# Optimization experiments

Hardware: AMD Instinct MI355X
Metric: run time of the kernel (lower is better)

The kernel has to match this reference:

```python
import jax, jax.numpy as jnp
import numpy as np

EPS = 1e-05


def layer_norm(x, scale):
    # Faithful to source bug: returns scale * x_norm + scale (shift param unused)
    mean = jnp.mean(x, axis=-1, keepdims=True)
    var = jnp.var(x, axis=-1, keepdims=True)  # unbiased=False
    x_norm = (x - mean) / jnp.sqrt(var + EPS)
    return scale * x_norm + scale


def mhsa(x, wq, wk, wv, wo, bo, n_heads):
    b, t, d = x.shape
    hd = d // n_heads
    # torch Linear: y = x @ W.T (no qkv bias)
    q = (x @ wq.T).reshape(b, t, n_heads, hd).transpose(0, 2, 1, 3)  # bhtd
    k = (x @ wk.T).reshape(b, t, n_heads, hd).transpose(0, 2, 1, 3)
    v = (x @ wv.T).reshape(b, t, n_heads, hd).transpose(0, 2, 1, 3)
    scores = jnp.einsum('bhqd,bhkd->bhqk', q, k)
    causal = jnp.triu(jnp.ones((t, t), dtype=bool), k=1)
    scores = jnp.where(causal, -jnp.inf, scores)
    attn = jax.nn.softmax(scores / np.sqrt(hd).astype(np.float32), axis=-1)
    ctx = jnp.einsum('bhqk,bhkd->bhqd', attn, v)
    ctx = ctx.transpose(0, 2, 1, 3).reshape(b, t, d)
    return ctx @ wo.T + bo


def setup_inputs() -> dict:
    key = jax.random.key(0)
    ks = jax.random.split(key, 6)
    B, T, D = 2, 2048, 1024
    return {
        'x': jax.random.normal(ks[0], (B, T, D), dtype=jnp.float32),
        'wq': jax.random.normal(ks[1], (D, D), dtype=jnp.float32) * 0.02,
        'wk': jax.random.normal(ks[2], (D, D), dtype=jnp.float32) * 0.02,
        'wv': jax.random.normal(ks[3], (D, D), dtype=jnp.float32) * 0.02,
        'wo': jax.random.normal(ks[4], (D, D), dtype=jnp.float32) * 0.02,
        'bo': jnp.zeros((D,), dtype=jnp.float32),
        'ln1_scale': jnp.ones((D,), dtype=jnp.float32),
        'ln2_scale': jnp.ones((D,), dtype=jnp.float32),
    }


def reference(x, wq, wk, wv, wo, bo, ln1_scale, ln2_scale):
    n_heads = 16
    # Block 1: norm1 -> attn -> (+residual); dropout is identity in eval mode
    h = x + mhsa(layer_norm(x, ln1_scale), wq, wk, wv, wo, bo, n_heads)
    # Block 2: source calls self.attn (same weights) again, not self.ff
    out = h + mhsa(layer_norm(h, ln2_scale), wq, wk, wv, wo, bo, n_heads)
    return out
```

## Files before the change

### kernel.cpp

```cpp
#include <hip/hip_runtime.h>
#include <hip/hip_bf16.h>
#include <math.h>

#define Dm 1024
#define Tm 2048
#define Bm 2
#define Hm 16
#define HDm 64
#define Rm (Bm*Tm)
#define QKS 2048

typedef __attribute__((ext_vector_type(8))) short sh8;
typedef __attribute__((ext_vector_type(4))) float f32x4;
typedef __attribute__((ext_vector_type(16))) float f32x16;

#define AS1(p) ((const __attribute__((address_space(1))) void*)(p))
#define AS3(p) ((__attribute__((address_space(3))) void*)(p))

__device__ __forceinline__ short f2bs(float f) {
    union { float f; unsigned u; } v; v.f = f;
    unsigned r = v.u + 0x7FFFu + ((v.u >> 16) & 1u);
    return (short)(r >> 16);
}

__global__ __launch_bounds__(256) void ln_conv(const float* __restrict__ x,
                                               const float* __restrict__ scale,
                                               short* __restrict__ out,
                                               const float* __restrict__ wq,
                                               const float* __restrict__ wk,
                                               const float* __restrict__ wv,
                                               const float* __restrict__ wo,
                                               short* __restrict__ wqkv,
                                               short* __restrict__ wob) {
    __shared__ float red[8];
    if (blockIdx.x >= 4096) {
        int idx = ((blockIdx.x - 4096) * 256 + threadIdx.x) * 4;
        const int M1 = 1 << 20;
        const float* src; short* dst; int off; float sc = 1.0f;
        if (idx < M1)           { src = wq; dst = wqkv;          off = idx; sc = 0.125f; }
        else if (idx < 2*M1)    { src = wk; dst = wqkv + M1;     off = idx - M1; }
        else if (idx < 3*M1)    { src = wv; dst = wqkv + 2*M1;   off = idx - 2*M1; }
        else                    { src = wo; dst = wob;           off = idx - 3*M1; }
        float4 v = *(const float4*)(src + off);
        short4 o;
        o.x = f2bs(v.x*sc); o.y = f2bs(v.y*sc); o.z = f2bs(v.z*sc); o.w = f2bs(v.w*sc);
        *(short4*)(dst + off) = o;
        return;
    }
    int row = blockIdx.x;
    int t = threadIdx.x;
    const float4* xr = (const float4*)(x + (size_t)row * Dm);
    float4 v = xr[t];
    float s  = v.x + v.y + v.z + v.w;
    float ss = v.x*v.x + v.y*v.y + v.z*v.z + v.w*v.w;
    #pragma unroll
    for (int off = 32; off; off >>= 1) {
        s  += __shfl_xor(s, off);
        ss += __shfl_xor(ss, off);
    }
    int wave = t >> 6, lane = t & 63;
    if (lane == 0) { red[wave*2] = s; red[wave*2+1] = ss; }
    __syncthreads();
    s  = red[0] + red[2] + red[4] + red[6];
    ss = red[1] + red[3] + red[5] + red[7];
    float mean = s * (1.0f / Dm);
    float var  = ss * (1.0f / Dm) - mean * mean;
    float rstd = 1.0f / sqrtf(var + 1e-5f);
    float4 sc = ((const float4*)scale)[t];
    short4 o;
    o.x = f2bs(sc.x * ((v.x - mean) * rstd) + sc.x);
    o.y = f2bs(sc.y * ((v.y - mean) * rstd) + sc.y);
    o.z = f2bs(sc.z * ((v.z - mean) * rstd) + sc.z);
    o.w = f2bs(sc.w * ((v.w - mean) * rstd) + sc.w);
    ((short4*)(out + (size_t)row * Dm))[t] = o;
}

__global__ __launch_bounds__(256) void ln_kernel(const float* __restrict__ x,
                                                 const float* __restrict__ scale,
                                                 short* __restrict__ out) {
    int row = blockIdx.x;
    int t = threadIdx.x;
    const float4* xr = (const float4*)(x + (size_t)row * Dm);
    float4 v = xr[t];
    float s  = v.x + v.y + v.z + v.w;
    float ss = v.x*v.x + v.y*v.y + v.z*v.z + v.w*v.w;
    #pragma unroll
    for (int off = 32; off; off >>= 1) {
        s  += __shfl_xor(s, off);
        ss += __shfl_xor(ss, off);
    }
    __shared__ float red[8];
    int wave = t >> 6, lane = t & 63;
    if (lane == 0) { red[wave*2] = s; red[wave*2+1] = ss; }
    __syncthreads();
    s  = red[0] + red[2] + red[4] + red[6];
    ss = red[1] + red[3] + red[5] + red[7];
    float mean = s * (1.0f / Dm);
    float var  = ss * (1.0f / Dm) - mean * mean;
    float rstd = 1.0f / sqrtf(var + 1e-5f);
    float4 sc = ((const float4*)scale)[t];
    short4 o;
    o.x = f2bs(sc.x * ((v.x - mean) * rstd) + sc.x);
    o.y = f2bs(sc.y * ((v.y - mean) * rstd) + sc.y);
    o.z = f2bs(sc.z * ((v.z - mean) * rstd) + sc.z);
    o.w = f2bs(sc.w * ((v.w - mean) * rstd) + sc.w);
    ((short4*)(out + (size_t)row * Dm))[t] = o;
}

template<int BN, int MODE>
__global__ __launch_bounds__(256) void gemm_mfma(const short* __restrict__ A,
                                                 const short* __restrict__ B,
                                                 const float* __restrict__ bias,
                                                 const float* __restrict__ res,
                                                 void* __restrict__ Cv,
                                                 short* __restrict__ Vt,
                                                 int M, int N, int K) {
    __shared__ short As[128*64];
    __shared__ short Bs[BN*64];
    __shared__ short Tb[(MODE==1) ? 4*16*68 : 4];
    const int NJ = BN / 32;
    int t = threadIdx.x;
    int lane = t & 63, w = t >> 6;
    int l = lane & 15, quad = lane >> 4;
    int wm = (w & 1) * 64, wn = (w >> 1) * (BN/2);
    int m0 = blockIdx.y * 128, n0 = blockIdx.x * BN;

    f32x4 acc[4][NJ];
    #pragma unroll
    for (int i = 0; i < 4; i++)
        #pragma unroll
        for (int j = 0; j < NJ; j++)
            acc[i][j] = (f32x4){0.f,0.f,0.f,0.f};

    for (int k0 = 0; k0 < K; k0 += 64) {
        __syncthreads();
        #pragma unroll
        for (int p = 0; p < 4; p++) {
            int off = p*4096 + t*16;
            int row = off >> 7;
            int c = ((off >> 4) & 7) ^ (row & 7);
            const short* ga = A + (size_t)(m0 + row) * K + k0 + c*8;
            __builtin_amdgcn_global_load_lds(AS1(ga), AS3((char*)As + off), 16, 0, 0);
        }
        #pragma unroll
        for (int p = 0; p < BN/32; p++) {
            int off = p*4096 + t*16;
            int row = off >> 7;
            int c = ((off >> 4) & 7) ^ (row & 7);
            const short* gb = B + (size_t)(n0 + row) * K + k0 + c*8;
            __builtin_amdgcn_global_load_lds(AS1(gb), AS3((char*)Bs + off), 16, 0, 0);
        }
        __syncthreads();
        sh8 a0[4], a1[4], b0[NJ], b1[NJ];
        #pragma unroll
        for (int i = 0; i < 4; i++) {
            int m = wm + i*16 + l;
            const char* ar = (const char*)As + m*128;
            int sw = m & 7;
            a0[i] = *(const sh8*)(ar + ((quad ^ sw) * 16));
            a1[i] = *(const sh8*)(ar + (((4 + quad) ^ sw) * 16));
        }
        #pragma unroll
        for (int j = 0; j < NJ; j++) {
            int n = wn + j*16 + l;
            const char* br = (const char*)Bs + n*128;
            int sw = n & 7;
            b0[j] = *(const sh8*)(br + ((quad ^ sw) * 16));
            b1[j] = *(const sh8*)(br + (((4 + quad) ^ sw) * 16));
        }
        #pragma unroll
        for (int i = 0; i < 4; i++)
            #pragma unroll
            for (int j = 0; j < NJ; j++) {
                acc[i][j] = __builtin_amdgcn_mfma_f32_16x16x32_bf16(a0[i], b0[j], acc[i][j], 0, 0, 0);
                acc[i][j] = __builtin_amdgcn_mfma_f32_16x16x32_bf16(a1[i], b1[j], acc[i][j], 0, 0, 0);
            }
    }
    if (MODE == 0) {
        #pragma unroll
        for (int i = 0; i < 4; i++)
            #pragma unroll
            for (int j = 0; j < NJ; j++)
                #pragma unroll
                for (int r = 0; r < 4; r++) {
                    int m = m0 + wm + i*16 + quad*4 + r;
                    int n = n0 + wn + j*16 + l;
                    float vv = acc[i][j][r] + bias[n] + res[(size_t)m * N + n];
                    ((float*)Cv)[(size_t)m * N + n] = vv;
                }
    } else {
        if (n0 < 2048) {
            #pragma unroll
            for (int i = 0; i < 4; i++)
                #pragma unroll
                for (int j = 0; j < NJ; j++)
                    #pragma unroll
                    for (int r = 0; r < 4; r++) {
                        int m = m0 + wm + i*16 + quad*4 + r;
                        int n = n0 + wn + j*16 + l;
                        ((short*)Cv)[(size_t)m * QKS + n] = f2bs(acc[i][j][r]);
                    }
        } else {
            int bq = m0 >> 11;
            int key0 = (m0 & 2047) + wm;
            int h = (n0 + wn - 2048) >> 6;
            int quad2 = ((quad & 1) << 1) | (quad >> 1);
            short* vout = Vt + ((size_t)(bq*Hm + h) * HDm) * Tm + key0;
            #pragma unroll
            for (int j = 0; j < NJ; j++) {
                #pragma unroll
                for (int i = 0; i < 4; i++) {
                    short4 o;
                    o.x = f2bs(acc[i][j][0]); o.y = f2bs(acc[i][j][1]);
                    o.z = f2bs(acc[i][j][2]); o.w = f2bs(acc[i][j][3]);
                    *(short4*)&Tb[w*(16*68) + l*68 + i*16 + quad2*4] = o;
                }
                #pragma unroll
                for (int st = 0; st < 2; st++) {
                    int rr = st*8 + (lane >> 3);
                    int cc = lane & 7;
                    sh8 vv = *(const sh8*)&Tb[w*(16*68) + rr*68 + cc*8];
                    *(sh8*)(vout + (size_t)(j*16 + rr) * Tm + cc*8) = vv;
                }
            }
        }
    }
}

__global__ __launch_bounds__(256) void attn_mfma(const short* __restrict__ qk,
                                                 const short* __restrict__ vtg,
                                                 short* __restrict__ ctx) {
    __shared__ short Kl[3][64*64];
    __shared__ short Vl[2][64*64];
    int t = threadIdx.x;
    int lane = t & 63, w = t >> 6;
    int qh = w & 1, kh = w >> 1;
    int l31 = lane & 31, hi = lane >> 5;
    int bh = blockIdx.x;
    int xi = blockIdx.y;
    int cc0 = xi & 7, kk0 = xi >> 3;
    int qt = (kk0 == 0) ? cc0 : (kk0 == 1) ? (15 - cc0)
           : (kk0 == 2) ? (16 + cc0) : (31 - cc0);
    int b = bh >> 4, h = bh & 15;
    size_t rbase = (size_t)b * Tm;
    const short* qp0 = qk + rbase * QKS + h*HDm;
    const short* kp0 = qp0 + Dm;
    const short* vh  = vtg + ((size_t)bh * HDm) * Tm;
    int qtbase = qt * 64;
    int qrow = qtbase + qh*32 + l31;

    sh8 qf[4];
    {
        const short* qp = qp0 + (size_t)qrow * QKS + hi*8;
        qf[0] = *(const sh8*)qp;
        qf[1] = *(const sh8*)(qp + 16);
        qf[2] = *(const sh8*)(qp + 32);
        qf[3] = *(const sh8*)(qp + 48);
    }

    f32x16 O0, O1;
    #pragma unroll
    for (int i = 0; i < 16; i++) { O0[i] = 0.f; O1[i] = 0.f; }
    float ps = 0.f;

    int trow = t >> 3;
    int c8 = ((t & 7) ^ (trow & 7)) * 8;
    int ldsoff = t * 16;
    const short* gkp = kp0 + (size_t)trow * QKS + c8;
    const short* gvp = vh + (size_t)trow * Tm + c8;

#define STAGE_K(KD) do { \
    __builtin_amdgcn_global_load_lds(AS1(gkp),                  AS3((char*)(KD) + ldsoff), 16, 0, 0); \
    __builtin_amdgcn_global_load_lds(AS1(gkp + (size_t)32*QKS), AS3((char*)(KD) + 4096 + ldsoff), 16, 0, 0); \
    gkp += (size_t)64*QKS; } while (0)

#define STAGE_V(VD) do { \
    __builtin_amdgcn_global_load_lds(AS1(gvp),                 AS3((char*)(VD) + ldsoff), 16, 0, 0); \
    __builtin_amdgcn_global_load_lds(AS1(gvp + (size_t)32*Tm), AS3((char*)(VD) + 4096 + ldsoff), 16, 0, 0); \
    gvp += 64; } while (0)

#define QKCOMP(KBUF) do { \
    const char* kr_ = (const char*)(KBUF) + (kh*32 + l31)*128; \
    int sw_ = l31 & 7; \
    f32x16 c_; \
    _Pragma("unroll") for (int i_ = 0; i_ < 16; i_++) c_[i_] = 0.f; \
    _Pragma("unroll") for (int s_ = 0; s_ < 4; s_++) { \
        sh8 kf_ = *(const sh8*)(kr_ + (((s_*2 + hi) ^ sw_) * 16)); \
        c_ = __builtin_amdgcn_mfma_f32_32x32x16_bf16(kf_, qf[s_], c_, 0, 0, 0); } \
    S0 = c_; \
} while (0)

    STAGE_K(Kl[0]);
    STAGE_V(Vl[0]);
    if (qt >= 1) STAGE_K(Kl[1]);
    __syncthreads();

    f32x16 S0;
    QKCOMP(Kl[0]);

    int bcur = 0;
    for (int kc = 0; kc <= qt; kc++) {
        int kbase = kc * 64;
        sh8 pa[2];
        {
            bool needmask = (kbase + kh*32 + 31 > qtbase + qh*32);
            float p_[16];
            if (needmask) {
                #pragma unroll
                for (int r = 0; r < 16; r++) {
                    int key_r = kbase + kh*32 + (r&3) + 8*(r>>2) + 4*hi;
                    p_[r] = (key_r > qrow) ? 0.f : __expf(S0[r]);
                }
            } else {
                #pragma unroll
                for (int r = 0; r < 16; r++) p_[r] = __expf(S0[r]);
            }
            ps += (((p_[0]+p_[1])+(p_[2]+p_[3])) + ((p_[4]+p_[5])+(p_[6]+p_[7])))
                + (((p_[8]+p_[9])+(p_[10]+p_[11])) + ((p_[12]+p_[13])+(p_[14]+p_[15])));
            #pragma unroll
            for (int gg = 0; gg < 2; gg++) {
                union { __hip_bfloat162 h2[4]; sh8 s8; } u;
                u.h2[0] = __float22bfloat162_rn({p_[gg*8+0], p_[gg*8+1]});
                u.h2[1] = __float22bfloat162_rn({p_[gg*8+2], p_[gg*8+3]});
                u.h2[2] = __float22bfloat162_rn({p_[gg*8+4], p_[gg*8+5]});
                u.h2[3] = __float22bfloat162_rn({p_[gg*8+6], p_[gg*8+7]});
                pa[gg] = u.s8;
            }
        }

        __syncthreads();

        int bnext = (bcur == 2) ? 0 : bcur + 1;
        if (kc + 2 <= qt) {
            int bnext2 = (bnext == 2) ? 0 : bnext + 1;
            STAGE_K(Kl[bnext2]);
        }
        if (kc + 1 <= qt) STAGE_V(Vl[(kc + 1) & 1]);

        if (kc < qt) QKCOMP(Kl[bnext]);

        const char* Vb = (const char*)Vl[kc & 1];
        int G0 = kh * 2;
        {
            const char* vr = Vb + l31*128;
            int sw = l31 & 7;
            sh8 v0 = *(const sh8*)(vr + ((((G0  )*2 + hi) ^ sw) * 16));
            sh8 v1 = *(const sh8*)(vr + ((((G0+1)*2 + hi) ^ sw) * 16));
            O0 = __builtin_amdgcn_mfma_f32_32x32x16_bf16(pa[0], v0, O0, 0, 0, 0);
            O0 = __builtin_amdgcn_mfma_f32_32x32x16_bf16(pa[1], v1, O0, 0, 0, 0);
        }
        {
            const char* vr = Vb + (32 + l31)*128;
            int sw = l31 & 7;
            sh8 v0 = *(const sh8*)(vr + ((((G0  )*2 + hi) ^ sw) * 16));
            sh8 v1 = *(const sh8*)(vr + ((((G0+1)*2 + hi) ^ sw) * 16));
            O1 = __builtin_amdgcn_mfma_f32_32x32x16_bf16(pa[0], v0, O1, 0, 0, 0);
            O1 = __builtin_amdgcn_mfma_f32_32x32x16_bf16(pa[1], v1, O1, 0, 0, 0);
        }
        bcur = bnext;
    }
#undef STAGE_K
#undef STAGE_V
#undef QKCOMP

    ps += __shfl_xor(ps, 32);
    __syncthreads();
    float* Lo  = (float*)Kl;
    float* Lps = (float*)Vl;
    if (kh == 1) {
        #pragma unroll
        for (int r = 0; r < 16; r++) {
            int rl = (r&3) + 8*(r>>2) + 4*hi;
            Lo[qh*2048 + rl*64 + l31]      = O0[r];
            Lo[qh*2048 + rl*64 + 32 + l31] = O1[r];
        }
        if (hi == 0) Lps[qh*32 + l31] = ps;
    }
    __syncthreads();
    if (kh == 0) {
        float pst = ps + Lps[qh*32 + l31];
        float inv_own = 1.0f / pst;
        short* cp = ctx + (rbase + qtbase + qh*32) * Dm + h*HDm + l31;
        #pragma unroll
        for (int r = 0; r < 16; r++) {
            int rl = (r&3) + 8*(r>>2) + 4*hi;
            float inv = __shfl(inv_own, rl);
            cp[(size_t)rl * Dm]      = f2bs((O0[r] + Lo[qh*2048 + rl*64 + l31]) * inv);
            cp[(size_t)rl * Dm + 32] = f2bs((O1[r] + Lo[qh*2048 + rl*64 + 32 + l31]) * inv);
        }
    }
}

extern "C" void kernel_launch(void* const* d_in, const int* in_sizes, int n_in,
                              void* d_out, int out_size, void* d_ws, size_t ws_size,
                              hipStream_t stream) {
    const float* x   = (const float*)d_in[0];
    const float* wq  = (const float*)d_in[1];
    const float* wk  = (const float*)d_in[2];
    const float* wv  = (const float*)d_in[3];
    const float* wo  = (const float*)d_in[4];
    const float* bo  = (const float*)d_in[5];
    const float* ln1 = (const float*)d_in[6];
    const float* ln2 = (const float*)d_in[7];
    float* out = (float*)d_out;

    short* lnb  = (short*)d_ws;
    short* ctxb = lnb  + (size_t)Rm*Dm;
    short* qk   = ctxb + (size_t)Rm*Dm;
    short* vtg  = qk   + (size_t)Rm*QKS;
    short* wqkv = vtg  + (size_t)Bm*Hm*HDm*Tm;
    short* wob  = wqkv + (size_t)3*Dm*Dm;

    dim3 qgrid(3072/128, Rm/128);
    dim3 pgrid(Dm/64,    Rm/128);
    dim3 agrid(32, 32);

    ln_conv<<<8192, 256, 0, stream>>>(x, ln1, lnb, wq, wk, wv, wo, wqkv, wob);
    gemm_mfma<128, 1><<<qgrid, 256, 0, stream>>>(lnb, wqkv, nullptr, nullptr, qk, vtg, Rm, 3072, Dm);
    attn_mfma<<<agrid, 256, 0, stream>>>(qk, vtg, ctxb);
    gemm_mfma<64, 0><<<pgrid, 256, 0, stream>>>(ctxb, wob, bo, x, out, nullptr, Rm, Dm, Dm);

    ln_kernel<<<Rm, 256, 0, stream>>>(out, ln2, lnb);
    gemm_mfma<128, 1><<<qgrid, 256, 0, stream>>>(lnb, wqkv, nullptr, nullptr, qk, vtg, Rm, 3072, Dm);
    attn_mfma<<<agrid, 256, 0, stream>>>(qk, vtg, ctxb);
    gemm_mfma<64, 0><<<pgrid, 256, 0, stream>>>(ctxb, wob, bo, out, out, nullptr, Rm, Dm, Dm);
}
```

Before: 266.8 us.

## Pair complementary causal query tiles per attention block for balanced work

```diff
diff --git a/kernel.cpp b/kernel.cpp
--- a/kernel.cpp
+++ b/kernel.cpp
@@ -231,31 +231,32 @@
                                                  const short* __restrict__ vtg,
                                                  short* __restrict__ ctx) {
     __shared__ short Kl[3][64*64];
-    __shared__ short Vl[2][64*64];
+    __shared__ short Vl[3][64*64];
+    __shared__ float Cb[2][32][64];
+    __shared__ float Cps[64];
     int t = threadIdx.x;
     int lane = t & 63, w = t >> 6;
     int qh = w & 1, kh = w >> 1;
     int l31 = lane & 31, hi = lane >> 5;
     int bh = blockIdx.x;
-    int xi = blockIdx.y;
-    int cc0 = xi & 7, kk0 = xi >> 3;
-    int qt = (kk0 == 0) ? cc0 : (kk0 == 1) ? (15 - cc0)
-           : (kk0 == 2) ? (16 + cc0) : (31 - cc0);
+    int pr = blockIdx.y;
+    int qt0 = pr, qt1 = 31 - pr;
     int b = bh >> 4, h = bh & 15;
     size_t rbase = (size_t)b * Tm;
     const short* qp0 = qk + rbase * QKS + h*HDm;
     const short* kp0 = qp0 + Dm;
     const short* vh  = vtg + ((size_t)bh * HDm) * Tm;
-    int qtbase = qt * 64;
-    int qrow = qtbase + qh*32 + l31;
-
-    sh8 qf[4];
+    int qrow0 = qt0*64 + qh*32 + l31;
+    int qrow1 = qt1*64 + qh*32 + l31;
+
+    sh8 qfA[4], qfB[4];
     {
-        const short* qp = qp0 + (size_t)qrow * QKS + hi*8;
-        qf[0] = *(const sh8*)qp;
-        qf[1] = *(const sh8*)(qp + 16);
-        qf[2] = *(const sh8*)(qp + 32);
-        qf[3] = *(const sh8*)(qp + 48);
+        const short* qp = qp0 + (size_t)qrow0 * QKS + hi*8;
+        qfA[0] = *(const sh8*)qp;       qfA[1] = *(const sh8*)(qp + 16);
+        qfA[2] = *(const sh8*)(qp + 32); qfA[3] = *(const sh8*)(qp + 48);
+        const short* qq = qp0 + (size_t)qrow1 * QKS + hi*8;
+        qfB[0] = *(const sh8*)qq;       qfB[1] = *(const sh8*)(qq + 16);
+        qfB[2] = *(const sh8*)(qq + 32); qfB[3] = *(const sh8*)(qq + 48);
     }
 
     f32x16 O0, O1;
@@ -266,49 +267,76 @@
     int trow = t >> 3;
     int c8 = ((t & 7) ^ (trow & 7)) * 8;
     int ldsoff = t * 16;
-    const short* gkp = kp0 + (size_t)trow * QKS + c8;
-    const short* gvp = vh + (size_t)trow * Tm + c8;
-
-#define STAGE_K(KD) do { \
-    __builtin_amdgcn_global_load_lds(AS1(gkp),                  AS3((char*)(KD) + ldsoff), 16, 0, 0); \
-    __builtin_amdgcn_global_load_lds(AS1(gkp + (size_t)32*QKS), AS3((char*)(KD) + 4096 + ldsoff), 16, 0, 0); \
-    gkp += (size_t)64*QKS; } while (0)
-
-#define STAGE_V(VD) do { \
-    __builtin_amdgcn_global_load_lds(AS1(gvp),                 AS3((char*)(VD) + ldsoff), 16, 0, 0); \
-    __builtin_amdgcn_global_load_lds(AS1(gvp + (size_t)32*Tm), AS3((char*)(VD) + 4096 + ldsoff), 16, 0, 0); \
-    gvp += 64; } while (0)
-
-#define QKCOMP(KBUF) do { \
+    const short* kst = kp0 + (size_t)trow * QKS + c8;
+    const short* vst = vh + (size_t)trow * Tm + c8;
+
+#define KBOF(j) ((((j) <= qt0) ? (j) : ((j) - qt0 - 1)) * 64)
+#define STAGE(j, rg) do { \
+    int kb_ = KBOF(j); \
+    const short* gk_ = kst + (size_t)kb_ * QKS; \
+    const short* gv_ = vst + kb_; \
+    __builtin_amdgcn_global_load_lds(AS1(gk_), AS3((char*)Kl[rg] + ldsoff), 16, 0, 0); \
+    __builtin_amdgcn_global_load_lds(AS1(gk_ + (size_t)32*QKS), AS3((char*)Kl[rg] + 4096 + ldsoff), 16, 0, 0); \
+    __builtin_amdgcn_global_load_lds(AS1(gv_), AS3((char*)Vl[rg] + ldsoff), 16, 0, 0); \
+    __builtin_amdgcn_global_load_lds(AS1(gv_ + (size_t)32*Tm), AS3((char*)Vl[rg] + 4096 + ldsoff), 16, 0, 0); \
+} while (0)
+
+#define QKCOMP(KBUF, QF) do { \
     const char* kr_ = (const char*)(KBUF) + (kh*32 + l31)*128; \
     int sw_ = l31 & 7; \
     f32x16 c_; \
     _Pragma("unroll") for (int i_ = 0; i_ < 16; i_++) c_[i_] = 0.f; \
     _Pragma("unroll") for (int s_ = 0; s_ < 4; s_++) { \
         sh8 kf_ = *(const sh8*)(kr_ + (((s_*2 + hi) ^ sw_) * 16)); \
-        c_ = __builtin_amdgcn_mfma_f32_32x32x16_bf16(kf_, qf[s_], c_, 0, 0, 0); } \
+        c_ = __builtin_amdgcn_mfma_f32_32x32x16_bf16(kf_, QF[s_], c_, 0, 0, 0); } \
     S0 = c_; \
 } while (0)
 
-    STAGE_K(Kl[0]);
-    STAGE_V(Vl[0]);
-    if (qt >= 1) STAGE_K(Kl[1]);
+#define EPI(QTB) do { \
+    ps += __shfl_xor(ps, 32); \
+    if (kh == 1) { \
+        _Pragma("unroll") for (int r_ = 0; r_ < 16; r_++) { \
+            int rl_ = (r_&3) + 8*(r_>>2) + 4*hi; \
+            Cb[qh][rl_][l31]      = O0[r_]; \
+            Cb[qh][rl_][32 + l31] = O1[r_]; \
+        } \
+        if (hi == 0) Cps[qh*32 + l31] = ps; \
+    } \
+    __syncthreads(); \
+    if (kh == 0) { \
+        float pst_ = ps + Cps[qh*32 + l31]; \
+        float invo_ = 1.0f / pst_; \
+        short* cp_ = ctx + (rbase + (QTB) + qh*32) * Dm + h*HDm + l31; \
+        _Pragma("unroll") for (int r_ = 0; r_ < 16; r_++) { \
+            int rl_ = (r_&3) + 8*(r_>>2) + 4*hi; \
+            float inv_ = __shfl(invo_, rl_); \
+            cp_[(size_t)rl_ * Dm]      = f2bs((O0[r_] + Cb[qh][rl_][l31]) * inv_); \
+            cp_[(size_t)rl_ * Dm + 32] = f2bs((O1[r_] + Cb[qh][rl_][32 + l31]) * inv_); \
+        } \
+    } \
+} while (0)
+
+    STAGE(0, 0);
+    STAGE(1, 1);
     __syncthreads();
 
     f32x16 S0;
-    QKCOMP(Kl[0]);
-
-    int bcur = 0;
-    for (int kc = 0; kc <= qt; kc++) {
-        int kbase = kc * 64;
+    QKCOMP(Kl[0], qfA);
+
+    for (int it = 0; it < 33; it++) {
+        int ph = (it <= qt0) ? 0 : 1;
+        int kb = KBOF(it);
+        int qtbase = ph ? qt1*64 : qt0*64;
+        int qrow = ph ? qrow1 : qrow0;
+
         sh8 pa[2];
         {
-            bool needmask = (kbase + kh*32 + 31 > qtbase + qh*32);
+            bool needmask = (kb + kh*32 + 31 > qtbase + qh*32);
             float p_[16];
             if (needmask) {
                 #pragma unroll
                 for (int r = 0; r < 16; r++) {
-                    int key_r = kbase + kh*32 + (r&3) + 8*(r>>2) + 4*hi;
+                    int key_r = kb + kh*32 + (r&3) + 8*(r>>2) + 4*hi;
                     p_[r] = (key_r > qrow) ? 0.f : __expf(S0[r]);
                 }
             } else {
@@ -330,16 +358,14 @@
 
         __syncthreads();
 
-        int bnext = (bcur == 2) ? 0 : bcur + 1;
-        if (kc + 2 <= qt) {
-            int bnext2 = (bnext == 2) ? 0 : bnext + 1;
-            STAGE_K(Kl[bnext2]);
-        }
-        if (kc + 1 <= qt) STAGE_V(Vl[(kc + 1) & 1]);
-
-        if (kc < qt) QKCOMP(Kl[bnext]);
-
-        const char* Vb = (const char*)Vl[kc & 1];
+        if (it + 2 < 33) STAGE(it + 2, (it + 2) % 3);
+
+        if (it + 1 < 33) {
+            if (it + 1 <= qt0) QKCOMP(Kl[(it + 1) % 3], qfA);
+            else               QKCOMP(Kl[(it + 1) % 3], qfB);
+        }
+
+        const char* Vb = (const char*)Vl[it % 3];
         int G0 = kh * 2;
         {
             const char* vr = Vb + l31*128;
@@ -357,38 +383,20 @@
             O1 = __builtin_amdgcn_mfma_f32_32x32x16_bf16(pa[0], v0, O1, 0, 0, 0);
             O1 = __builtin_amdgcn_mfma_f32_32x32x16_bf16(pa[1], v1, O1, 0, 0, 0);
         }
-        bcur = bnext;
-    }
-#undef STAGE_K
-#undef STAGE_V
+
+        if (it == qt0) {
+            EPI(qt0*64);
+            #pragma unroll
+            for (int i = 0; i < 16; i++) { O0[i] = 0.f; O1[i] = 0.f; }
+            ps = 0.f;
+        }
+    }
+
+    EPI(qt1*64);
+#undef KBOF
+#undef STAGE
 #undef QKCOMP
-
-    ps += __shfl_xor(ps, 32);
-    __syncthreads();
-    float* Lo  = (float*)Kl;
-    float* Lps = (float*)Vl;
-    if (kh == 1) {
-        #pragma unroll
-        for (int r = 0; r < 16; r++) {
-            int rl = (r&3) + 8*(r>>2) + 4*hi;
-            Lo[qh*2048 + rl*64 + l31]      = O0[r];
-            Lo[qh*2048 + rl*64 + 32 + l31] = O1[r];
-        }
-        if (hi == 0) Lps[qh*32 + l31] = ps;
-    }
-    __syncthreads();
-    if (kh == 0) {
-        float pst = ps + Lps[qh*32 + l31];
-        float inv_own = 1.0f / pst;
-        short* cp = ctx + (rbase + qtbase + qh*32) * Dm + h*HDm + l31;
-        #pragma unroll
-        for (int r = 0; r < 16; r++) {
-            int rl = (r&3) + 8*(r>>2) + 4*hi;
-            float inv = __shfl(inv_own, rl);
-            cp[(size_t)rl * Dm]      = f2bs((O0[r] + Lo[qh*2048 + rl*64 + l31]) * inv);
-            cp[(size_t)rl * Dm + 32] = f2bs((O1[r] + Lo[qh*2048 + rl*64 + 32 + l31]) * inv);
-        }
-    }
+#undef EPI
 }
 
 extern "C" void kernel_launch(void* const* d_in, const int* in_sizes, int n_in,
@@ -413,7 +421,7 @@
 
     dim3 qgrid(3072/128, Rm/128);
     dim3 pgrid(Dm/64,    Rm/128);
-    dim3 agrid(32, 32);
+    dim3 agrid(32, 16);
 
     ln_conv<<<8192, 256, 0, stream>>>(x, ln1, lnb, wq, wk, wv, wo, wqkv, wob);
     gemm_mfma<128, 1><<<qgrid, 256, 0, stream>>>(lnb, wqkv, nullptr, nullptr, qk, vtg, Rm, 3072, Dm);
```

Measured after the change: 283.1 us. 6.1% more time.

## Double-buffer LDS tiles in MFMA GEMM to overlap loads with compute

Applied to the files above, without the earlier changes.

```diff
diff --git a/kernel.cpp b/kernel.cpp
--- a/kernel.cpp
+++ b/kernel.cpp
@@ -115,9 +115,9 @@
                                                  void* __restrict__ Cv,
                                                  short* __restrict__ Vt,
                                                  int M, int N, int K) {
-    __shared__ short As[128*64];
-    __shared__ short Bs[BN*64];
-    __shared__ short Tb[(MODE==1) ? 4*16*68 : 4];
+    __shared__ short As[2][128*64];
+    __shared__ short Bs[2][BN*64];
+    short* Tb = (short*)As;
     const int NJ = BN / 32;
     int t = threadIdx.x;
     int lane = t & 63, w = t >> 6;
@@ -132,30 +132,37 @@
         for (int j = 0; j < NJ; j++)
             acc[i][j] = (f32x4){0.f,0.f,0.f,0.f};
 
-    for (int k0 = 0; k0 < K; k0 += 64) {
-        __syncthreads();
-        #pragma unroll
-        for (int p = 0; p < 4; p++) {
-            int off = p*4096 + t*16;
-            int row = off >> 7;
-            int c = ((off >> 4) & 7) ^ (row & 7);
-            const short* ga = A + (size_t)(m0 + row) * K + k0 + c*8;
-            __builtin_amdgcn_global_load_lds(AS1(ga), AS3((char*)As + off), 16, 0, 0);
-        }
-        #pragma unroll
-        for (int p = 0; p < BN/32; p++) {
-            int off = p*4096 + t*16;
-            int row = off >> 7;
-            int c = ((off >> 4) & 7) ^ (row & 7);
-            const short* gb = B + (size_t)(n0 + row) * K + k0 + c*8;
-            __builtin_amdgcn_global_load_lds(AS1(gb), AS3((char*)Bs + off), 16, 0, 0);
-        }
-        __syncthreads();
+#define GSTAGE(k0_, buf_) do { \
+    _Pragma("unroll") \
+    for (int p_ = 0; p_ < 4; p_++) {              \
+        int off_ = p_*4096 + t*16; \
+        int row_ = off_ >> 7; \
+        int c_ = ((off_ >> 4) & 7) ^ (row_ & 7); \
+        const short* ga_ = A + (size_t)(m0 + row_) * K + (k0_) + c_*8; \
+        __builtin_amdgcn_global_load_lds(AS1(ga_), AS3((char*)As[buf_] + off_), 16, 0, 0); \
+    } \
+    _Pragma("unroll") \
+    for (int p_ = 0; p_ < BN/32; p_++) {          \
+        int off_ = p_*4096 + t*16; \
+        int row_ = off_ >> 7; \
+        int c_ = ((off_ >> 4) & 7) ^ (row_ & 7); \
+        const short* gb_ = B + (size_t)(n0 + row_) * K + (k0_) + c_*8; \
+        __builtin_amdgcn_global_load_lds(AS1(gb_), AS3((char*)Bs[buf_] + off_), 16, 0, 0); \
+    } \
+} while (0)
+
+    const int NK = 16;
+    GSTAGE(0, 0);
+    __syncthreads();
+    for (int ks = 0; ks < NK; ks++) {
+        int cur = ks & 1;
+        if (ks + 1 < NK) GSTAGE((ks + 1) * 64, cur ^ 1);
+
         sh8 a0[4], a1[4], b0[NJ], b1[NJ];
         #pragma unroll
         for (int i = 0; i < 4; i++) {
             int m = wm + i*16 + l;
-            const char* ar = (const char*)As + m*128;
+            const char* ar = (const char*)As[cur] + m*128;
             int sw = m & 7;
             a0[i] = *(const sh8*)(ar + ((quad ^ sw) * 16));
             a1[i] = *(const sh8*)(ar + (((4 + quad) ^ sw) * 16));
@@ -163,7 +170,7 @@
         #pragma unroll
         for (int j = 0; j < NJ; j++) {
             int n = wn + j*16 + l;
-            const char* br = (const char*)Bs + n*128;
+            const char* br = (const char*)Bs[cur] + n*128;
             int sw = n & 7;
             b0[j] = *(const sh8*)(br + ((quad ^ sw) * 16));
             b1[j] = *(const sh8*)(br + (((4 + quad) ^ sw) * 16));
@@ -175,7 +182,10 @@
                 acc[i][j] = __builtin_amdgcn_mfma_f32_16x16x32_bf16(a0[i], b0[j], acc[i][j], 0, 0, 0);
                 acc[i][j] = __builtin_amdgcn_mfma_f32_16x16x32_bf16(a1[i], b1[j], acc[i][j], 0, 0, 0);
             }
-    }
+        __syncthreads();
+    }
+#undef GSTAGE
+
     if (MODE == 0) {
         #pragma unroll
         for (int i = 0; i < 4; i++)
```

Measured after the change: 299.8 us. 1.12x slower.
